# Kernel tuning notes

Hardware: AMD Instinct MI355X
Metric: run time of the kernel (lower is better)

Reference implementation:

```python
import jax, jax.numpy as jnp
import numpy as np

N = 100000
E = 1600000
F_IN, H = 64, 128


def setup_inputs() -> dict:
    key = jax.random.key(0)
    ks = jax.random.split(key, 8)
    inp = {
        "x": jax.random.normal(ks[0], (N, F_IN), dtype=jnp.float32),
        "edge_index": jax.random.randint(ks[1], (2, E), 0, N, dtype=jnp.int64),
        "W1": jax.random.normal(ks[2], (F_IN, H), dtype=jnp.float32) / np.sqrt(F_IN),
        "b1": jnp.zeros((H,), jnp.float32),
        "W2": jax.random.normal(ks[3], (H, H), dtype=jnp.float32) / np.sqrt(H),
        "b2": jnp.zeros((H,), jnp.float32),
        "W3": jax.random.normal(ks[4], (H, H // 2), dtype=jnp.float32) / np.sqrt(H),
        "b3": jnp.zeros((H // 2,), jnp.float32),
        "Wc1": jax.random.normal(ks[5], (H // 2, H // 4), dtype=jnp.float32) / np.sqrt(H // 2),
        "bc1": jnp.zeros((H // 4,), jnp.float32),
        "Wc2": jax.random.normal(ks[6], (H // 4, 2), dtype=jnp.float32) / np.sqrt(H // 4),
        "bc2": jnp.zeros((2,), jnp.float32),
    }
    return inp


def _gcn_norm(edge_index, n):
    # PyG GCNConv default: add self-loops, symmetric D^-1/2 A_hat D^-1/2 norm
    loop = jnp.arange(n, dtype=edge_index.dtype)
    src = jnp.concatenate([edge_index[0], loop])
    dst = jnp.concatenate([edge_index[1], loop])
    deg = jax.ops.segment_sum(jnp.ones_like(dst, dtype=jnp.float32), dst, num_segments=n)
    dis = jax.lax.rsqrt(jnp.maximum(deg, 1.0))
    norm = dis[src] * dis[dst]  # [E+N]
    return src, dst, norm


def _gcn_conv(x, W, b, src, dst, norm, n):
    h = x @ W                      # [N, H_out]
    msg = h[src] * norm[:, None]   # gather + scale, [E+N, H_out]
    out = jax.ops.segment_sum(msg, dst, num_segments=n)  # scatter-add
    return out + b


def reference(x, edge_index, W1, b1, W2, b2, W3, b3, Wc1, bc1, Wc2, bc2):
    n = x.shape[0]
    src, dst, norm = _gcn_norm(edge_index, n)
    h1 = jax.nn.relu(_gcn_conv(x, W1, b1, src, dst, norm, n))
    h2 = jax.nn.relu(_gcn_conv(h1, W2, b2, src, dst, norm, n))
    h3 = jax.nn.relu(_gcn_conv(h2, W3, b3, src, dst, norm, n))
    pooled = jnp.mean(h3, axis=0, keepdims=True)  # [1, H//2]
    z = jax.nn.relu(pooled @ Wc1 + bc1)
    logits = z @ Wc2 + bc2
    return jax.nn.softmax(logits, axis=1)
```

## Files before the change

kernel.cpp:

```cpp
#include <hip/hip_runtime.h>

#define NN 100000
#define NE 1600000
#define NBUCKET 391
#define CHUNK 4096

typedef __attribute__((ext_vector_type(2))) float v2f;
typedef __attribute__((ext_vector_type(8))) short bf16x8;
typedef __attribute__((ext_vector_type(4))) float f32x4;


__device__ __forceinline__ unsigned int pk4fp8(float a, float b, float c, float d) {
    int t = __builtin_amdgcn_cvt_pk_fp8_f32(a, b, 0, false);
    t = __builtin_amdgcn_cvt_pk_fp8_f32(c, d, t, true);
    return (unsigned int)t;
}
__device__ __forceinline__ void acc4(unsigned int u, float* a) {
    v2f p0 = __builtin_amdgcn_cvt_pk_f32_fp8((int)u, false);
    v2f p1 = __builtin_amdgcn_cvt_pk_f32_fp8((int)u, true);
    a[0] += p0.x; a[1] += p0.y; a[2] += p1.x; a[3] += p1.y;
}
__device__ __forceinline__ void acc16(uint4 u, float* a) {
    acc4(u.x, a); acc4(u.y, a + 4); acc4(u.z, a + 8); acc4(u.w, a + 12);
}


__device__ __forceinline__ unsigned short f2b(float f) {
    unsigned int u; __builtin_memcpy(&u, &f, 4);
    unsigned int r = (u + 0x7fffu + ((u >> 16) & 1u)) >> 16;
    return (unsigned short)r;
}
__device__ __forceinline__ unsigned int pk2b(float a, float b) {
    return (unsigned int)f2b(a) | ((unsigned int)f2b(b) << 16);
}

__global__ __launch_bounds__(256) void k_init(
    const float* __restrict__ W1, const float* __restrict__ W2,
    const float* __restrict__ W3, uint4* __restrict__ Wp,
    int* __restrict__ bcnt, int* __restrict__ done_cnt) {
    int t = blockIdx.x * 256 + threadIdx.x;
    if (t < 4096) {
        const float* W; int Dout, e, base;
        if (t < 1024)       { W = W1; Dout = 128; e = t;        base = 0; }
        else if (t < 3072)  { W = W2; Dout = 128; e = t - 1024; base = 1024; }
        else                { W = W3; Dout = 64;  e = t - 3072; base = 3072; }
        int k4q = e / Dout, ch = e % Dout;
        int k0 = (k4q >> 2) * 32 + (k4q & 3) * 8;
        float v[8];
        #pragma unroll
        for (int j = 0; j < 8; j++) v[j] = W[(k0 + j) * Dout + ch];
        uint4 u;
        u.x = pk2b(v[0], v[1]); u.y = pk2b(v[2], v[3]);
        u.z = pk2b(v[4], v[5]); u.w = pk2b(v[6], v[7]);
        Wp[base + e] = u;
    } else {
        int i = t - 4096;
        if (i < NBUCKET) bcnt[i] = 0;
        if (i == NBUCKET) { done_cnt[0] = 0; done_cnt[1] = 0; }
    }
}


__global__ __launch_bounds__(256) void k_p1(const int* __restrict__ dst,
                                            int* __restrict__ bcnt, int E) {
    __shared__ int h[NBUCKET];
    for (int i = threadIdx.x; i < NBUCKET; i += 256) h[i] = 0;
    __syncthreads();
    int stride = gridDim.x * 256;
    for (int i = blockIdx.x * 256 + threadIdx.x; i < E; i += stride)
        atomicAdd(&h[dst[i] >> 8], 1);
    __syncthreads();
    for (int i = threadIdx.x; i < NBUCKET; i += 256)
        if (h[i]) atomicAdd(&bcnt[i], h[i]);
}

__global__ void k_scanb(const int* __restrict__ bcnt, int* __restrict__ bbase,
                        int* __restrict__ bfill) {
    __shared__ int s[512];
    int t = threadIdx.x;
    int v = (t < NBUCKET) ? bcnt[t] : 0;
    s[t] = v; __syncthreads();
    for (int off = 1; off < 512; off <<= 1) {
        int x = (t >= off) ? s[t - off] : 0;
        __syncthreads();
        s[t] += x;
        __syncthreads();
    }
    if (t < NBUCKET) { int ex = s[t] - v; bbase[t] = ex; bfill[t] = ex; }
    if (t == NBUCKET) bbase[t] = s[511];
}

__global__ __launch_bounds__(256) void k_p2(const int* __restrict__ src,
                                            const int* __restrict__ dst,
                                            int* __restrict__ bfill,
                                            unsigned int* __restrict__ entries, int E) {
    __shared__ int h[NBUCKET];
    __shared__ int cur[NBUCKET];
    int c0 = blockIdx.x * CHUNK;
    int c1 = min(E, c0 + CHUNK);
    for (int i = threadIdx.x; i < NBUCKET; i += 256) h[i] = 0;
    __syncthreads();
    for (int i = c0 + threadIdx.x; i < c1; i += 256) atomicAdd(&h[dst[i] >> 8], 1);
    __syncthreads();
    for (int i = threadIdx.x; i < NBUCKET; i += 256)
        cur[i] = h[i] ? atomicAdd(&bfill[i], h[i]) : 0;
    __syncthreads();
    for (int i = c0 + threadIdx.x; i < c1; i += 256) {
        int d = dst[i];
        int bkt = d >> 8;
        int pos = atomicAdd(&cur[bkt], 1);
        entries[pos] = (unsigned int)src[i] | ((unsigned int)(d & 255) << 17);
    }
}

__global__ __launch_bounds__(256) void k_p4x(const unsigned int* __restrict__ entries,
                                             const int* __restrict__ bbase,
                                             int* __restrict__ row_ptr,
                                             float* __restrict__ dis,
                                             int* __restrict__ col,
                                             const float4* __restrict__ x4,
                                             uint2* __restrict__ xb2, int N) {
    __shared__ int cnt[256];
    __shared__ int cur[256];
    __shared__ int sc[256];
    __shared__ float sdis[256];
    int b = blockIdx.x;
    int e0 = bbase[b], e1 = bbase[b + 1];
    int t = threadIdx.x;
    cnt[t] = 0; __syncthreads();
    for (int i = e0 + t; i < e1; i += 256)
        atomicAdd(&cnt[(entries[i] >> 17) & 255], 1);
    __syncthreads();
    int v = cnt[t];
    sc[t] = v; __syncthreads();
    for (int off = 1; off < 256; off <<= 1) {
        int x = (t >= off) ? sc[t - off] : 0;
        __syncthreads();
        sc[t] += x;
        __syncthreads();
    }
    int ex = sc[t] - v;
    int n = (b << 8) + t;
    float dv = rsqrtf((float)(v + 1));
    if (n <= N) row_ptr[n] = e0 + ex;
    if (n < N) dis[n] = dv;
    sdis[t] = dv;
    cur[t] = e0 + ex;
    __syncthreads();
    for (int i = e0 + t; i < e1; i += 256) {
        unsigned int en = entries[i];
        int pos = atomicAdd(&cur[(en >> 17) & 255], 1);
        col[pos] = (int)(en & 0x1FFFF);
    }
    for (int idx = t; idx < 256 * 8; idx += 256) {
        int node = idx >> 3, k = idx & 7;
        int gn = (b << 8) + node;
        if (gn < N) {
            float s = sdis[node];
            float4 A = x4[gn * 16 + 2 * k];
            float4 B = x4[gn * 16 + 2 * k + 1];
            uint2 u;
            u.x = pk4fp8(A.x * s, A.y * s, A.z * s, A.w * s);
            u.y = pk4fp8(B.x * s, B.y * s, B.z * s, B.w * s);
            xb2[gn * 8 + k] = u;
        }
    }
}

__global__ __launch_bounds__(256) void k_l1f(
    const uint4* __restrict__ xb4, const int* __restrict__ row_ptr,
    const int* __restrict__ col, const float* __restrict__ dis,
    const uint4* __restrict__ Wp, const float* __restrict__ b1,
    unsigned int* __restrict__ h1u, int N) {
    __shared__ unsigned short lds[4][16][72];
    const int tid = threadIdx.x, lane = tid & 63, wave = tid >> 6;
    const int slot = lane >> 2, seg = lane & 3;
    const int n = blockIdx.x * 64 + wave * 16 + slot;
    float a[16];
    #pragma unroll
    for (int q = 0; q < 16; q++) a[q] = 0.f;
    if (n < N) {
        int b = row_ptr[n], e = row_ptr[n + 1];
        acc16(xb4[n * 4 + seg], a);
        int i = b;
        for (; i + 4 <= e; i += 4) {
            int c0 = col[i], c1 = col[i + 1], c2 = col[i + 2], c3 = col[i + 3];
            uint4 u0 = xb4[c0 * 4 + seg], u1 = xb4[c1 * 4 + seg];
            uint4 u2 = xb4[c2 * 4 + seg], u3 = xb4[c3 * 4 + seg];
            acc16(u0, a); acc16(u1, a); acc16(u2, a); acc16(u3, a);
        }
        for (; i < e; i++) acc16(xb4[col[i] * 4 + seg], a);
        float s = dis[n];
        #pragma unroll
        for (int q = 0; q < 16; q++) a[q] *= s;
    }
    uint4 u0, u1;
    u0.x = pk2b(a[0],  a[1]);  u0.y = pk2b(a[2],  a[3]);
    u0.z = pk2b(a[4],  a[5]);  u0.w = pk2b(a[6],  a[7]);
    u1.x = pk2b(a[8],  a[9]);  u1.y = pk2b(a[10], a[11]);
    u1.z = pk2b(a[12], a[13]); u1.w = pk2b(a[14], a[15]);
    *(uint4*)&lds[wave][slot][seg * 16]     = u0;
    *(uint4*)&lds[wave][slot][seg * 16 + 8] = u1;
    __syncthreads();
    const int quad = lane >> 4, l16 = lane & 15;
    const int node = blockIdx.x * 64 + wave * 16 + l16;
    const bool valid = node < N;
    bf16x8 bfrag[2];
    #pragma unroll
    for (int kt = 0; kt < 2; kt++)
        bfrag[kt] = *(bf16x8*)&lds[wave][l16][kt * 32 + quad * 8];
    const float s2 = valid ? dis[node] : 0.f;
    #pragma unroll
    for (int ct = 0; ct < 8; ct++) {
        f32x4 c = {0.f, 0.f, 0.f, 0.f};
        #pragma unroll
        for (int kt = 0; kt < 2; kt++) {
            uint4 wu = Wp[(kt * 4 + quad) * 128 + ct * 16 + l16];
            c = __builtin_amdgcn_mfma_f32_16x16x32_bf16(*(bf16x8*)&wu, bfrag[kt], c, 0, 0, 0);
        }
        if (valid) {
            const int chb = ct * 16 + quad * 4;
            float r0 = fmaxf(c[0] + b1[chb + 0], 0.f) * s2;
            float r1 = fmaxf(c[1] + b1[chb + 1], 0.f) * s2;
            float r2 = fmaxf(c[2] + b1[chb + 2], 0.f) * s2;
            float r3 = fmaxf(c[3] + b1[chb + 3], 0.f) * s2;
            h1u[(size_t)node * 32 + ct * 4 + quad] = pk4fp8(r0, r1, r2, r3);
        }
    }
}

__global__ __launch_bounds__(256) void k_l2f(
    const uint4* __restrict__ h1b4, const int* __restrict__ row_ptr,
    const int* __restrict__ col, const float* __restrict__ dis,
    const uint4* __restrict__ Wp2, const uint4* __restrict__ Wp3,
    const float* __restrict__ b2,
    unsigned int* __restrict__ g3u, int N) {
    __shared__ unsigned short lds[4][16][136];
    const int tid = threadIdx.x, lane = tid & 63, wave = tid >> 6;
    const int slot = lane >> 3, seg = lane & 7;
    #pragma unroll
    for (int j = 0; j < 2; j++) {
        const int nl = wave * 16 + j * 8 + slot;
        const int n = blockIdx.x * 64 + nl;
        float a[16];
        #pragma unroll
        for (int q = 0; q < 16; q++) a[q] = 0.f;
        if (n < N) {
            int b = row_ptr[n], e = row_ptr[n + 1];
            acc16(h1b4[(size_t)n * 8 + seg], a);
            int i = b;
            for (; i + 4 <= e; i += 4) {
                int c0 = col[i], c1 = col[i + 1], c2 = col[i + 2], c3 = col[i + 3];
                uint4 u0 = h1b4[(size_t)c0 * 8 + seg], u1 = h1b4[(size_t)c1 * 8 + seg];
                uint4 u2 = h1b4[(size_t)c2 * 8 + seg], u3 = h1b4[(size_t)c3 * 8 + seg];
                acc16(u0, a); acc16(u1, a); acc16(u2, a); acc16(u3, a);
            }
            for (; i < e; i++) acc16(h1b4[(size_t)col[i] * 8 + seg], a);
            float s = dis[n];
            #pragma unroll
            for (int q = 0; q < 16; q++) a[q] *= s;
        }
        uint4 u0, u1;
        u0.x = pk2b(a[0],  a[1]);  u0.y = pk2b(a[2],  a[3]);
        u0.z = pk2b(a[4],  a[5]);  u0.w = pk2b(a[6],  a[7]);
        u1.x = pk2b(a[8],  a[9]);  u1.y = pk2b(a[10], a[11]);
        u1.z = pk2b(a[12], a[13]); u1.w = pk2b(a[14], a[15]);
        const int lnl = j * 8 + slot;
        *(uint4*)&lds[wave][lnl][seg * 16]     = u0;
        *(uint4*)&lds[wave][lnl][seg * 16 + 8] = u1;
    }
    __syncthreads();
    const int quad = lane >> 4, l16 = lane & 15;
    const int node = blockIdx.x * 64 + wave * 16 + l16;
    const bool valid = node < N;
    bf16x8 bfrag[4];
    #pragma unroll
    for (int kt = 0; kt < 4; kt++)
        bfrag[kt] = *(bf16x8*)&lds[wave][l16][kt * 32 + quad * 8];
    const float s = valid ? dis[node] : 0.f;
    #pragma unroll
    for (int ct = 0; ct < 8; ct++) {
        f32x4 c = {0.f, 0.f, 0.f, 0.f};
        #pragma unroll
        for (int kt = 0; kt < 4; kt++) {
            uint4 wu = Wp2[(kt * 4 + quad) * 128 + ct * 16 + l16];
            c = __builtin_amdgcn_mfma_f32_16x16x32_bf16(*(bf16x8*)&wu, bfrag[kt], c, 0, 0, 0);
        }
        const int chb = ct * 16 + quad * 4;
        float r0 = fmaxf(c[0] + b2[chb + 0], 0.f) * s;
        float r1 = fmaxf(c[1] + b2[chb + 1], 0.f) * s;
        float r2 = fmaxf(c[2] + b2[chb + 2], 0.f) * s;
        float r3 = fmaxf(c[3] + b2[chb + 3], 0.f) * s;
        uint2 u; u.x = pk2b(r0, r1); u.y = pk2b(r2, r3);
        *(uint2*)&lds[wave][l16][chb] = u;
    }
    __syncthreads();
    bf16x8 b2frag[4];
    #pragma unroll
    for (int kt = 0; kt < 4; kt++)
        b2frag[kt] = *(bf16x8*)&lds[wave][l16][kt * 32 + quad * 8];
    #pragma unroll
    for (int ct = 0; ct < 4; ct++) {
        f32x4 c = {0.f, 0.f, 0.f, 0.f};
        #pragma unroll
        for (int kt = 0; kt < 4; kt++) {
            uint4 wu = Wp3[(kt * 4 + quad) * 64 + ct * 16 + l16];
            c = __builtin_amdgcn_mfma_f32_16x16x32_bf16(*(bf16x8*)&wu, b2frag[kt], c, 0, 0, 0);
        }
        if (valid)
            g3u[(size_t)node * 16 + ct * 4 + quad] = pk4fp8(c[0], c[1], c[2], c[3]);
    }
}

__global__ __launch_bounds__(256) void k_aggpools(
    const uint4* __restrict__ g4, const int* __restrict__ row_ptr,
    const int* __restrict__ col, const float* __restrict__ dis,
    const float* __restrict__ b3, float* __restrict__ partial, int N) {
    int tid = threadIdx.x;
    int lane = tid & 63, wave = tid >> 6;
    int slot = lane >> 2, seg = lane & 3;
    int n = blockIdx.x * 64 + wave * 16 + slot;
    float ap[16];
    #pragma unroll
    for (int j = 0; j < 16; j++) ap[j] = 0.f;
    if (n < N) {
        int b = row_ptr[n], e = row_ptr[n + 1];
        float a[16];
        #pragma unroll
        for (int q = 0; q < 16; q++) a[q] = 0.f;
        acc16(g4[n * 4 + seg], a);
        int i = b;
        for (; i + 4 <= e; i += 4) {
            int c0 = col[i], c1 = col[i + 1], c2 = col[i + 2], c3 = col[i + 3];
            uint4 u0 = g4[c0 * 4 + seg], u1 = g4[c1 * 4 + seg];
            uint4 u2 = g4[c2 * 4 + seg], u3 = g4[c3 * 4 + seg];
            acc16(u0, a); acc16(u1, a); acc16(u2, a); acc16(u3, a);
        }
        for (; i < e; i++) acc16(g4[col[i] * 4 + seg], a);
        float s = dis[n];
        #pragma unroll
        for (int j = 0; j < 16; j++)
            ap[j] = fmaxf(s * a[j] + b3[seg * 16 + j], 0.f);
    }
    #pragma unroll
    for (int j = 0; j < 16; j++) {
        ap[j] += __shfl_xor(ap[j], 4);
        ap[j] += __shfl_xor(ap[j], 8);
        ap[j] += __shfl_xor(ap[j], 16);
        ap[j] += __shfl_xor(ap[j], 32);
    }
    __shared__ float red[4][64];
    if (slot == 0) {
        #pragma unroll
        for (int j = 0; j < 16; j++) red[wave][seg * 16 + j] = ap[j];
    }
    __syncthreads();
    if (tid < 64)
        partial[blockIdx.x * 64 + tid] =
            red[0][tid] + red[1][tid] + red[2][tid] + red[3][tid];
}

__global__ __launch_bounds__(256) void k_redhead(
    const float* __restrict__ partial, float* __restrict__ partial2,
    const float* __restrict__ Wc1, const float* __restrict__ bc1,
    const float* __restrict__ Wc2, const float* __restrict__ bc2,
    float* __restrict__ out, int* __restrict__ done_cnt,
    int NB, int NRED, float invN) {
    __shared__ float red[256];
    __shared__ float pooled[64];
    __shared__ float z[32];
    __shared__ float lg[2];
    __shared__ int isLast;
    int blk = blockIdx.x, t = threadIdx.x;
    int lane = t & 63, grp = t >> 6;
    int start = blk * 16, end = min(NB, start + 16);
    float s = 0.f;
    for (int b = start + grp; b < end; b += 4) s += partial[b * 64 + lane];
    red[t] = s; __syncthreads();
    if (t < 64)
        partial2[blk * 64 + t] = red[t] + red[t + 64] + red[t + 128] + red[t + 192];
    __threadfence();
    if (t == 0) isLast = (atomicAdd(done_cnt, 1) == NRED - 1);
    __syncthreads();
    if (!isLast) return;
    __threadfence();
    float s2 = 0.f;
    for (int b = grp; b < NRED; b += 4) s2 += partial2[b * 64 + lane];
    red[t] = s2; __syncthreads();
    if (t < 64) pooled[t] = (red[t] + red[t + 64] + red[t + 128] + red[t + 192]) * invN;
    __syncthreads();
    if (t < 32) {
        float a = bc1[t];
        for (int l = 0; l < 64; l++) a += pooled[l] * Wc1[l * 32 + t];
        z[t] = fmaxf(a, 0.f);
    }
    __syncthreads();
    if (t < 2) {
        float a = bc2[t];
        for (int j = 0; j < 32; j++) a += z[j] * Wc2[j * 2 + t];
        lg[t] = a;
    }
    __syncthreads();
    if (t == 0) {
        float m = fmaxf(lg[0], lg[1]);
        float e0 = __expf(lg[0] - m), e1 = __expf(lg[1] - m);
        float inv = 1.f / (e0 + e1);
        out[0] = e0 * inv;
        out[1] = e1 * inv;
    }
}


extern "C" void kernel_launch(void* const* d_in, const int* in_sizes, int n_in,
                              void* d_out, int out_size, void* d_ws, size_t ws_size,
                              hipStream_t stream) {
    (void)in_sizes; (void)n_in; (void)out_size; (void)ws_size;
    const int N = NN, E = NE;

    const float* x   = (const float*)d_in[0];
    const int*   ei  = (const int*)d_in[1];
    const int*   srcp = ei;
    const int*   dstp = ei + E;
    const float* W1 = (const float*)d_in[2];
    const float* b1 = (const float*)d_in[3];
    const float* W2 = (const float*)d_in[4];
    const float* b2 = (const float*)d_in[5];
    const float* W3 = (const float*)d_in[6];
    const float* b3 = (const float*)d_in[7];
    const float* Wc1 = (const float*)d_in[8];
    const float* bc1 = (const float*)d_in[9];
    const float* Wc2 = (const float*)d_in[10];
    const float* bc2 = (const float*)d_in[11];
    float* out = (float*)d_out;

    char* base = (char*)d_ws;
    size_t off = 0;
    auto carve = [&](size_t bytes) -> char* {
        char* p = base + off;
        off = (off + bytes + 255) & ~(size_t)255;
        return p;
    };
    int*   bcnt    = (int*)carve((size_t)NBUCKET * 4);
    int*   bbase   = (int*)carve((size_t)(NBUCKET + 1) * 4);
    int*   bfill   = (int*)carve((size_t)NBUCKET * 4);
    int*   done_cnt= (int*)carve(256);
    int*   row_ptr = (int*)carve((size_t)(N + 1) * 4);
    int*   col     = (int*)carve((size_t)E * 4);
    float* dis     = (float*)carve((size_t)N * 4);
    float* partial = (float*)carve((size_t)1600 * 64 * 4);
    float* partial2= (float*)carve((size_t)128 * 64 * 4);
    uint4* Wp      = (uint4*)carve((size_t)4096 * 16);
    unsigned int* entries = (unsigned int*)carve((size_t)E * 4);
    unsigned int* xb      = (unsigned int*)carve((size_t)N * 64);
    unsigned int* h1u     = (unsigned int*)carve((size_t)N * 128);
    unsigned int* g3u     = (unsigned int*)carve((size_t)N * 64);

    k_init<<<18, 256, 0, stream>>>(W1, W2, W3, Wp, bcnt, done_cnt);
    k_p1<<<512, 256, 0, stream>>>(dstp, bcnt, E);
    k_scanb<<<1, 512, 0, stream>>>(bcnt, bbase, bfill);
    k_p2<<<(E + CHUNK - 1) / CHUNK, 256, 0, stream>>>(srcp, dstp, bfill, entries, E);
    k_p4x<<<NBUCKET, 256, 0, stream>>>(entries, bbase, row_ptr, dis, col,
                                       (const float4*)x, (uint2*)xb, N);

    const int NB64 = (N + 63) / 64;

    k_l1f<<<NB64, 256, 0, stream>>>((const uint4*)xb, row_ptr, col, dis, Wp, b1, h1u, N);

    k_l2f<<<NB64, 256, 0, stream>>>((const uint4*)h1u, row_ptr, col, dis,
                                    Wp + 1024, Wp + 3072, b2, g3u, N);

    k_aggpools<<<NB64, 256, 0, stream>>>((const uint4*)g3u, row_ptr, col, dis, b3, partial, N);

    const int NRED = (NB64 + 15) / 16;
    k_redhead<<<NRED, 256, 0, stream>>>(partial, partial2, Wc1, bc1, Wc2, bc2,
                                        out, &done_cnt[1], NB64, NRED, 1.0f / (float)N);
}
```

Baseline: 283.5 us.

## Process nodes in degree-sorted order to balance per-wave aggregation work

Builds a degree histogram in the CSR build kernel, scans it in a last-block pass, and adds a counting-sort kernel that writes a permutation of nodes grouped by in-degree. The three aggregation kernels then read nodes through this permutation so that lanes in a wave have similar neighbour counts, reducing divergence in the gather loops. In exchange there is an extra kernel launch, an extra indirection per node, and a loss of locality between consecutive nodes' self-feature reads and output writes.

```diff
diff --git a/kernel.cpp b/kernel.cpp
--- a/kernel.cpp
+++ b/kernel.cpp
@@ -37,7 +37,8 @@
 __global__ __launch_bounds__(256) void k_init(
     const float* __restrict__ W1, const float* __restrict__ W2,
     const float* __restrict__ W3, uint4* __restrict__ Wp,
-    int* __restrict__ bcnt, int* __restrict__ done_cnt) {
+    int* __restrict__ bcnt, int* __restrict__ done_cnt,
+    int* __restrict__ degcnt) {
     int t = blockIdx.x * 256 + threadIdx.x;
     if (t < 4096) {
         const float* W; int Dout, e, base;
@@ -56,7 +57,8 @@
     } else {
         int i = t - 4096;
         if (i < NBUCKET) bcnt[i] = 0;
-        if (i == NBUCKET) { done_cnt[0] = 0; done_cnt[1] = 0; }
+        if (i >= NBUCKET && i < NBUCKET + 2) done_cnt[i - NBUCKET] = 0;
+        if (i >= NBUCKET + 2 && i < NBUCKET + 2 + 64) degcnt[i - NBUCKET - 2] = 0;
     }
 }
 
@@ -119,15 +121,23 @@
                                              float* __restrict__ dis,
                                              int* __restrict__ col,
                                              const float4* __restrict__ x4,
-                                             uint2* __restrict__ xb2, int N) {
+                                             uint2* __restrict__ xb2,
+                                             int* __restrict__ degcnt,
+                                             int* __restrict__ degbase,
+                                             int* __restrict__ degfill,
+                                             int* __restrict__ done_cnt, int N) {
     __shared__ int cnt[256];
     __shared__ int cur[256];
     __shared__ int sc[256];
     __shared__ float sdis[256];
+    __shared__ int d64[64];
+    __shared__ int isLast;
     int b = blockIdx.x;
     int e0 = bbase[b], e1 = bbase[b + 1];
     int t = threadIdx.x;
-    cnt[t] = 0; __syncthreads();
+    cnt[t] = 0;
+    if (t < 64) d64[t] = 0;
+    __syncthreads();
     for (int i = e0 + t; i < e1; i += 256)
         atomicAdd(&cnt[(entries[i] >> 17) & 255], 1);
     __syncthreads();
@@ -143,10 +153,11 @@
     int n = (b << 8) + t;
     float dv = rsqrtf((float)(v + 1));
     if (n <= N) row_ptr[n] = e0 + ex;
-    if (n < N) dis[n] = dv;
+    if (n < N) { dis[n] = dv; atomicAdd(&d64[min(v, 63)], 1); }
     sdis[t] = dv;
     cur[t] = e0 + ex;
     __syncthreads();
+    if (t < 64 && d64[t]) atomicAdd(&degcnt[t], d64[t]);
     for (int i = e0 + t; i < e1; i += 256) {
         unsigned int en = entries[i];
         int pos = atomicAdd(&cur[(en >> 17) & 255], 1);
@@ -165,21 +176,59 @@
             xb2[gn * 8 + k] = u;
         }
     }
+    __threadfence();
+    if (t == 0) isLast = (atomicAdd(done_cnt, 1) == (int)gridDim.x - 1);
+    __syncthreads();
+    if (!isLast) return;
+    __threadfence();
+    __shared__ int ds[64];
+    if (t < 64) ds[t] = degcnt[t];
+    __syncthreads();
+    if (t == 0) {
+        int run = 0;
+        for (int i = 0; i < 64; i++) { int x = ds[i]; ds[i] = run; run += x; }
+    }
+    __syncthreads();
+    if (t < 64) { degbase[t] = ds[t]; degfill[t] = ds[t]; }
+}
+
+__global__ __launch_bounds__(256) void k_perm(
+    const int* __restrict__ row_ptr, int* __restrict__ degfill,
+    int* __restrict__ perm, int N) {
+    __shared__ int hist[64];
+    __shared__ int base[64];
+    __shared__ int cur[64];
+    int t = threadIdx.x;
+    int n = blockIdx.x * 256 + t;
+    int bin = -1;
+    if (n < N) bin = min(row_ptr[n + 1] - row_ptr[n], 63);
+    if (t < 64) hist[t] = 0;
+    __syncthreads();
+    if (bin >= 0) atomicAdd(&hist[bin], 1);
+    __syncthreads();
+    if (t < 64) { base[t] = hist[t] ? atomicAdd(&degfill[t], hist[t]) : 0; cur[t] = 0; }
+    __syncthreads();
+    if (bin >= 0) {
+        int r = atomicAdd(&cur[bin], 1);
+        perm[base[bin] + r] = n;
+    }
 }
 
 __global__ __launch_bounds__(256) void k_l1f(
     const uint4* __restrict__ xb4, const int* __restrict__ row_ptr,
     const int* __restrict__ col, const float* __restrict__ dis,
+    const int* __restrict__ perm,
     const uint4* __restrict__ Wp, const float* __restrict__ b1,
     unsigned int* __restrict__ h1u, int N) {
     __shared__ unsigned short lds[4][16][72];
     const int tid = threadIdx.x, lane = tid & 63, wave = tid >> 6;
     const int slot = lane >> 2, seg = lane & 3;
-    const int n = blockIdx.x * 64 + wave * 16 + slot;
+    const int pos = blockIdx.x * 64 + wave * 16 + slot;
     float a[16];
     #pragma unroll
     for (int q = 0; q < 16; q++) a[q] = 0.f;
-    if (n < N) {
+    if (pos < N) {
+        const int n = perm[pos];
         int b = row_ptr[n], e = row_ptr[n + 1];
         acc16(xb4[n * 4 + seg], a);
         int i = b;
@@ -203,8 +252,9 @@
     *(uint4*)&lds[wave][slot][seg * 16 + 8] = u1;
     __syncthreads();
     const int quad = lane >> 4, l16 = lane & 15;
-    const int node = blockIdx.x * 64 + wave * 16 + l16;
-    const bool valid = node < N;
+    const int pos2 = blockIdx.x * 64 + wave * 16 + l16;
+    const bool valid = pos2 < N;
+    const int node = valid ? perm[pos2] : 0;
     bf16x8 bfrag[2];
     #pragma unroll
     for (int kt = 0; kt < 2; kt++)
@@ -232,6 +282,7 @@
 __global__ __launch_bounds__(256) void k_l2f(
     const uint4* __restrict__ h1b4, const int* __restrict__ row_ptr,
     const int* __restrict__ col, const float* __restrict__ dis,
+    const int* __restrict__ perm,
     const uint4* __restrict__ Wp2, const uint4* __restrict__ Wp3,
     const float* __restrict__ b2,
     unsigned int* __restrict__ g3u, int N) {
@@ -240,12 +291,13 @@
     const int slot = lane >> 3, seg = lane & 7;
     #pragma unroll
     for (int j = 0; j < 2; j++) {
-        const int nl = wave * 16 + j * 8 + slot;
-        const int n = blockIdx.x * 64 + nl;
+        const int lnl = j * 8 + slot;
+        const int pos = blockIdx.x * 64 + wave * 16 + lnl;
         float a[16];
         #pragma unroll
         for (int q = 0; q < 16; q++) a[q] = 0.f;
-        if (n < N) {
+        if (pos < N) {
+            const int n = perm[pos];
             int b = row_ptr[n], e = row_ptr[n + 1];
             acc16(h1b4[(size_t)n * 8 + seg], a);
             int i = b;
@@ -265,14 +317,14 @@
         u0.z = pk2b(a[4],  a[5]);  u0.w = pk2b(a[6],  a[7]);
         u1.x = pk2b(a[8],  a[9]);  u1.y = pk2b(a[10], a[11]);
         u1.z = pk2b(a[12], a[13]); u1.w = pk2b(a[14], a[15]);
-        const int lnl = j * 8 + slot;
         *(uint4*)&lds[wave][lnl][seg * 16]     = u0;
         *(uint4*)&lds[wave][lnl][seg * 16 + 8] = u1;
     }
     __syncthreads();
     const int quad = lane >> 4, l16 = lane & 15;
-    const int node = blockIdx.x * 64 + wave * 16 + l16;
-    const bool valid = node < N;
+    const int pos2 = blockIdx.x * 64 + wave * 16 + l16;
+    const bool valid = pos2 < N;
+    const int node = valid ? perm[pos2] : 0;
     bf16x8 bfrag[4];
     #pragma unroll
     for (int kt = 0; kt < 4; kt++)
@@ -315,15 +367,17 @@
 __global__ __launch_bounds__(256) void k_aggpools(
     const uint4* __restrict__ g4, const int* __restrict__ row_ptr,
     const int* __restrict__ col, const float* __restrict__ dis,
+    const int* __restrict__ perm,
     const float* __restrict__ b3, float* __restrict__ partial, int N) {
     int tid = threadIdx.x;
     int lane = tid & 63, wave = tid >> 6;
     int slot = lane >> 2, seg = lane & 3;
-    int n = blockIdx.x * 64 + wave * 16 + slot;
+    int pos = blockIdx.x * 64 + wave * 16 + slot;
     float ap[16];
     #pragma unroll
     for (int j = 0; j < 16; j++) ap[j] = 0.f;
-    if (n < N) {
+    if (pos < N) {
+        const int n = perm[pos];
         int b = row_ptr[n], e = row_ptr[n + 1];
         float a[16];
         #pragma unroll
@@ -444,9 +498,13 @@
     int*   bbase   = (int*)carve((size_t)(NBUCKET + 1) * 4);
     int*   bfill   = (int*)carve((size_t)NBUCKET * 4);
     int*   done_cnt= (int*)carve(256);
+    int*   degcnt  = (int*)carve(64 * 4);
+    int*   degbase = (int*)carve(65 * 4);
+    int*   degfill = (int*)carve(64 * 4);
     int*   row_ptr = (int*)carve((size_t)(N + 1) * 4);
     int*   col     = (int*)carve((size_t)E * 4);
     float* dis     = (float*)carve((size_t)N * 4);
+    int*   perm    = (int*)carve((size_t)N * 4);
     float* partial = (float*)carve((size_t)1600 * 64 * 4);
     float* partial2= (float*)carve((size_t)128 * 64 * 4);
     uint4* Wp      = (uint4*)carve((size_t)4096 * 16);
@@ -455,21 +513,25 @@
     unsigned int* h1u     = (unsigned int*)carve((size_t)N * 128);
     unsigned int* g3u     = (unsigned int*)carve((size_t)N * 64);
 
-    k_init<<<18, 256, 0, stream>>>(W1, W2, W3, Wp, bcnt, done_cnt);
+    k_init<<<18, 256, 0, stream>>>(W1, W2, W3, Wp, bcnt, done_cnt, degcnt);
     k_p1<<<512, 256, 0, stream>>>(dstp, bcnt, E);
     k_scanb<<<1, 512, 0, stream>>>(bcnt, bbase, bfill);
     k_p2<<<(E + CHUNK - 1) / CHUNK, 256, 0, stream>>>(srcp, dstp, bfill, entries, E);
     k_p4x<<<NBUCKET, 256, 0, stream>>>(entries, bbase, row_ptr, dis, col,
-                                       (const float4*)x, (uint2*)xb, N);
+                                       (const float4*)x, (uint2*)xb,
+                                       degcnt, degbase, degfill, &done_cnt[0], N);
+    k_perm<<<NBUCKET, 256, 0, stream>>>(row_ptr, degfill, perm, N);
 
     const int NB64 = (N + 63) / 64;
 
-    k_l1f<<<NB64, 256, 0, stream>>>((const uint4*)xb, row_ptr, col, dis, Wp, b1, h1u, N);
-
-    k_l2f<<<NB64, 256, 0, stream>>>((const uint4*)h1u, row_ptr, col, dis,
+    k_l1f<<<NB64, 256, 0, stream>>>((const uint4*)xb, row_ptr, col, dis, perm,
+                                    Wp, b1, h1u, N);
+
+    k_l2f<<<NB64, 256, 0, stream>>>((const uint4*)h1u, row_ptr, col, dis, perm,
                                     Wp + 1024, Wp + 3072, b2, g3u, N);
 
-    k_aggpools<<<NB64, 256, 0, stream>>>((const uint4*)g3u, row_ptr, col, dis, b3, partial, N);
+    k_aggpools<<<NB64, 256, 0, stream>>>((const uint4*)g3u, row_ptr, col, dis, perm,
+                                         b3, partial, N);
 
     const int NRED = (NB64 + 15) / 16;
     k_redhead<<<NRED, 256, 0, stream>>>(partial, partial2, Wc1, bc1, Wc2, bc2,
```

After: 345.9 us. +22.0%, slower.
